# Kernel optimization log

Measured on AMD Instinct MI355X. Metric: run time of the kernel, lower is better.

## Reference

```python
import jax, jax.numpy as jnp
import numpy as np

B, N = 4, 512
C_IN, H, W = 1024, 48, 48
IMG_H, IMG_W = 48.0, 48.0
CNN_EMB, BOX_EMB, GCN_OUT = 512, 256, 512
ROWS, COLS = 58, 30
ALPHA = 5.0
K_EDGES = 8 * N  # edges kept per image per graph

# all directed pairs (i != j) of a fully-connected graph on N nodes
_ii, _jj = np.meshgrid(np.arange(N), np.arange(N), indexing='ij')
_m = _ii != _jj
PAIRS = jnp.asarray(np.stack([_ii[_m], _jj[_m]], axis=1).astype(np.int32))  # [E,2]


def setup_inputs():
    key = jax.random.key(0)
    ks = jax.random.split(key, 12)
    x = jax.random.normal(ks[0], (B, C_IN, H, W), jnp.float32)
    # valid boxes (x1<x2, y1<y2) inside the 48x48 feature map
    p = jax.random.uniform(ks[1], (B, N, 2, 2), minval=0.0, maxval=float(W) - 2.0)
    lo = jnp.min(p, axis=2)
    hi = jnp.max(p, axis=2) + 1.0
    boxes = jnp.concatenate([lo, hi], axis=-1)  # [B,N,4] x1,y1,x2,y2

    def lin(k, fi, fo):
        return jax.random.normal(k, (fi, fo), jnp.float32) / np.sqrt(fi)

    return {
        'input': x, 'boxes': boxes,
        'im_scales': jnp.ones((B,), jnp.float32),
        'pdls': jnp.zeros((B,), jnp.float32),
        'pdts': jnp.zeros((B,), jnp.float32),
        'W_dec': jax.random.normal(ks[2], (256, C_IN, 3, 3), jnp.float32) / np.sqrt(C_IN * 9.0),
        'b_dec': jnp.zeros((256,), jnp.float32),
        'W_box': lin(ks[3], 4, BOX_EMB), 'b_box': jnp.zeros((BOX_EMB,), jnp.float32),
        'W_cnn': lin(ks[4], 256 * 4, CNN_EMB), 'b_cnn': jnp.zeros((CNN_EMB,), jnp.float32),
        'W_grow': lin(ks[5], CNN_EMB + BOX_EMB, GCN_OUT), 'b_grow': jnp.zeros((GCN_OUT,), jnp.float32),
        'W_gcol': lin(ks[6], CNN_EMB + BOX_EMB, GCN_OUT), 'b_gcol': jnp.zeros((GCN_OUT,), jnp.float32),
        'W_rcls': lin(ks[7], GCN_OUT, 2 * (ROWS - 1) * 2), 'b_rcls': jnp.zeros((2 * (ROWS - 1) * 2,), jnp.float32),
        'W_ccls': lin(ks[8], GCN_OUT, 2 * (COLS - 1) * 2), 'b_ccls': jnp.zeros((2 * (COLS - 1) * 2,), jnp.float32),
    }


def _bilinear(feat, bidx, py, px):
    # feat [B,C,H,W]; py,px [M,4] sample coords -> [M,4,C]
    Hh, Ww = feat.shape[2], feat.shape[3]
    py = jnp.clip(py, 0.0, Hh - 1.0)
    px = jnp.clip(px, 0.0, Ww - 1.0)
    y0 = jnp.floor(py).astype(jnp.int32)
    x0 = jnp.floor(px).astype(jnp.int32)
    y1 = jnp.minimum(y0 + 1, Hh - 1)
    x1 = jnp.minimum(x0 + 1, Ww - 1)
    wy = (py - y0)[..., None]
    wx = (px - x0)[..., None]
    b = bidx[:, None]
    f00 = feat[b, :, y0, x0]
    f01 = feat[b, :, y0, x1]
    f10 = feat[b, :, y1, x0]
    f11 = feat[b, :, y1, x1]
    return f00 * (1 - wy) * (1 - wx) + f01 * (1 - wy) * wx + f10 * wy * (1 - wx) + f11 * wy * wx


def _roi_align_2x2(feat, boxes, bidx):
    # roi_align output_size=2, spatial_scale=1, one sample per bin (bin center)
    x1, y1, x2, y2 = boxes[:, 0], boxes[:, 1], boxes[:, 2], boxes[:, 3]
    bw = (x2 - x1) / 2.0
    bh = (y2 - y1) / 2.0
    offs = jnp.array([0.5, 1.5], jnp.float32)
    sx = x1[:, None] + offs * bw[:, None]  # [M,2]
    sy = y1[:, None] + offs * bh[:, None]
    py = sy[:, jnp.array([0, 0, 1, 1])]  # (iy, ix) ordering
    px = sx[:, jnp.array([0, 1, 0, 1])]
    val = _bilinear(feat, bidx, py, px)  # [M,4,C]
    return jnp.transpose(val, (0, 2, 1)).reshape(val.shape[0], -1)  # [M, C*2*2]


def _edge_attrs(boxes_i, scale, pdl, pdt):
    org = (boxes_i - jnp.stack([pdl, pdt, pdl, pdt])) / scale
    cx = (org[:, 0] + org[:, 2]) * 0.5
    cy = (org[:, 1] + org[:, 3]) * 0.5
    tb_w = jnp.max(org[:, jnp.array([0, 2])])
    tb_h = jnp.max(org[:, jnp.array([1, 3])])
    s, d = PAIRS[:, 0], PAIRS[:, 1]
    row_attr = jnp.exp(-jnp.square((cy[s] - cy[d]) * ALPHA / tb_h))
    col_attr = jnp.exp(-jnp.square((cx[s] - cx[d]) * ALPHA / tb_w))
    rv, ri = jax.lax.top_k(row_attr, K_EDGES)
    cv, ci = jax.lax.top_k(col_attr, K_EDGES)
    return rv, PAIRS[ri], cv, PAIRS[ci]


def _gcn(x, Wg, bg, edges, ew, num_nodes):
    # PyG GCNConv: self-loops with weight 1, symmetric normalization
    loop = jnp.arange(num_nodes, dtype=edges.dtype)
    src = jnp.concatenate([edges[0], loop])
    dst = jnp.concatenate([edges[1], loop])
    w = jnp.concatenate([ew, jnp.ones((num_nodes,), ew.dtype)])
    deg = jax.ops.segment_sum(w, dst, num_segments=num_nodes)
    dis = jax.lax.rsqrt(deg)  # deg >= 1 thanks to self-loops
    norm = dis[src] * w * dis[dst]
    xw = x @ Wg
    agg = jax.ops.segment_sum(norm[:, None] * xw[src], dst, num_segments=num_nodes)
    return agg + bg


def _forward(input, boxes, im_scales, pdls, pdts, W_dec, b_dec, W_box, b_box,
             W_cnn, b_cnn, W_grow, b_grow, W_gcol, b_gcol, W_rcls, b_rcls, W_ccls, b_ccls):
    Bn = B * N
    flat = boxes.reshape(Bn, 4)
    # box features (relative center / size)
    cx = (flat[:, 0] + flat[:, 2]) / 2.0
    cy = (flat[:, 1] + flat[:, 3]) / 2.0
    bf = jnp.stack([cx / IMG_W, cy / IMG_H,
                    (flat[:, 2] - flat[:, 0]) / IMG_W,
                    (flat[:, 3] - flat[:, 1]) / IMG_H], axis=1)
    box_feat = jax.nn.relu(bf @ W_box + b_box)
    # decode conv + relu
    dec = jax.lax.conv_general_dilated(input, W_dec, (1, 1), 'SAME',
                                       dimension_numbers=('NCHW', 'OIHW', 'NCHW'))
    dec = jax.nn.relu(dec + b_dec[None, :, None, None])
    # roi-align 2x2 + cnn embedding
    bidx = jnp.repeat(jnp.arange(B, dtype=jnp.int32), N)
    cnn = _roi_align_2x2(dec, flat, bidx)
    cnn_feat = jax.nn.relu(cnn @ W_cnn + b_cnn)
    # per-image dense graph -> top-8N row/col edges
    rv, re, cv, ce = jax.vmap(_edge_attrs)(boxes, im_scales, pdls, pdts)
    off = (jnp.arange(B, dtype=jnp.int32) * N)[:, None, None]
    row_edge = (re + off).reshape(-1, 2).T  # [2, B*K]
    col_edge = (ce + off).reshape(-1, 2).T
    row_w = rv.reshape(-1)
    col_w = cv.reshape(-1)
    fusion = jnp.concatenate([box_feat, cnn_feat], axis=1)  # [Bn, 768]
    row_feat = jax.nn.relu(_gcn(fusion, W_grow, b_grow, row_edge, row_w, Bn))
    col_feat = jax.nn.relu(_gcn(fusion, W_gcol, b_gcol, col_edge, col_w, Bn))
    row_score = jax.nn.leaky_relu(row_feat @ W_rcls + b_rcls, 0.01).reshape(Bn, 2, ROWS - 1, 2)
    col_score = jax.nn.leaky_relu(col_feat @ W_ccls + b_ccls, 0.01).reshape(Bn, 2, COLS - 1, 2)
    return row_score, col_score


def reference(input, boxes, im_scales, pdls, pdts, W_dec, b_dec, W_box, b_box,
              W_cnn, b_cnn, W_grow, b_grow, W_gcol, b_gcol, W_rcls, b_rcls, W_ccls, b_ccls):
    return _forward(input, boxes, im_scales, pdls, pdts, W_dec, b_dec, W_box, b_box,
                    W_cnn, b_cnn, W_grow, b_grow, W_gcol, b_gcol,
                    W_rcls, b_rcls, W_ccls, b_ccls)
```

## Files before the change

### kernel.cpp

```cpp
#include <hip/hip_runtime.h>
#include <cstdint>
#include <math.h>

typedef unsigned int u32;
typedef unsigned long long u64;
typedef unsigned short ushort;

typedef __attribute__((ext_vector_type(8))) _Float16 f16x8;
typedef __attribute__((ext_vector_type(4))) _Float16 f16x4;
typedef __attribute__((ext_vector_type(4))) float f32x4;

#define NB    4
#define BnN   2048
#define NE    261632
#define NCHUNK 16
#define ECHUNK 16352
#define KEDGE 4096
#define TIECAP 2048
#define PSLICE 2359296
#define MS    64
#define TS    64

__global__ __launch_bounds__(256) void cvt_x_kernel(
    const float* __restrict__ in, _Float16* __restrict__ xf)
{
    __shared__ _Float16 sh[64][49];
    int cg = blockIdx.x, y = blockIdx.y, b = blockIdx.z;
    int tid = threadIdx.x;
    for (int i = tid; i < 64 * 48; i += 256) {
        int cl = i / 48, x = i - cl * 48;
        sh[cl][x] = (_Float16)in[(((size_t)b * 1024 + cg * 64 + cl) * 48 + y) * 48 + x];
    }
    __syncthreads();
    for (int i = tid; i < 64 * 48; i += 256) {
        int x = i / 64, cl = i - x * 64;
        xf[((size_t)(b * 48 + y) * 48 + x) * 1024 + cg * 64 + cl] = sh[cl][x];
    }
}

__global__ __launch_bounds__(256) void cvt_w_kernel(
    const float* __restrict__ W, _Float16* __restrict__ wf)
{
    __shared__ _Float16 sh[9216];
    int o = blockIdx.x, tid = threadIdx.x;
    for (int g = tid; g < 9216; g += 256)
        sh[g] = (_Float16)W[(size_t)o * 9216 + g];
    __syncthreads();
    for (int g = tid; g < 9216; g += 256) {
        int tap = g >> 10, ch = g & 1023;
        wf[(size_t)o * 9216 + g] = sh[ch * 9 + tap];
    }
}

__global__ __launch_bounds__(256) void cvt_t5_kernel(
    const float* __restrict__ Wc,  _Float16* __restrict__ WcT,
    const float* __restrict__ Wgr, _Float16* __restrict__ WgrT,
    const float* __restrict__ Wgc, _Float16* __restrict__ WgcT,
    const float* __restrict__ Wr,  _Float16* __restrict__ WrT,
    const float* __restrict__ Wcc, _Float16* __restrict__ WccT)
{
    __shared__ _Float16 sh[32][33];
    int bid = blockIdx.x;
    const float* in; _Float16* out; int K, N, tx0, ty0, ntx;
    if (bid < 512)       { in = Wc;  out = WcT;  K = 1024; N = 512; ntx = 16; bid -= 0;    }
    else if (bid < 896)  { in = Wgr; out = WgrT; K = 768;  N = 512; ntx = 16; bid -= 512;  }
    else if (bid < 1280) { in = Wgc; out = WgcT; K = 768;  N = 512; ntx = 16; bid -= 896;  }
    else if (bid < 1408) { in = Wr;  out = WrT;  K = 512;  N = 228; ntx = 8;  bid -= 1280; }
    else                 { in = Wcc; out = WccT; K = 512;  N = 116; ntx = 4;  bid -= 1408; }
    tx0 = (bid % ntx) * 32;
    ty0 = (bid / ntx) * 32;
    int tx = threadIdx.x & 31, ty = threadIdx.x >> 5;
#pragma unroll
    for (int i = 0; i < 4; ++i) {
        int k = ty0 + ty + i * 8, n = tx0 + tx;
        sh[ty + i * 8][tx] = (k < K && n < N) ? (_Float16)in[(size_t)k * N + n] : (_Float16)0.f;
    }
    __syncthreads();
#pragma unroll
    for (int i = 0; i < 4; ++i) {
        int n = tx0 + ty + i * 8, k = ty0 + tx;
        if (n < N && k < K) out[(size_t)n * K + k] = sh[tx][ty + i * 8];
    }
}

__global__ __launch_bounds__(256) void conv_part_kernel(
    const _Float16* __restrict__ xf, const _Float16* __restrict__ wf,
    float* __restrict__ pbuf)
{
    __shared__ _Float16 wS[9][4][32][8];
    __shared__ _Float16 xS[10][4][50][8];
    const int y0 = blockIdx.x * 8;
    const int og = blockIdx.y;
    const int bz = blockIdx.z;
    const int b  = bz >> 2, ks = bz & 3;
    const int tid = threadIdx.x;
    const int wv = tid >> 6;
    const int ln = tid & 63;
    const int n  = ln & 15;
    const int q  = ln >> 4;

    f32x4 acc[2][2][3];
#pragma unroll
    for (int mt = 0; mt < 2; ++mt)
#pragma unroll
        for (int rr = 0; rr < 2; ++rr)
#pragma unroll
            for (int nt = 0; nt < 3; ++nt) acc[mt][rr][nt] = (f32x4){0.f, 0.f, 0.f, 0.f};

    const int c0 = ks * 256;
    for (int cc = c0; cc < c0 + 256; cc += 32) {
#pragma unroll
        for (int it = 0; it < 5; ++it) {
            int g = it * 256 + tid;
            if (g < 1152) {
                int tap = g >> 7, r = g & 127, qq = r >> 5, oc = r & 31;
                *(uint4*)&wS[tap][qq][oc][0] =
                    *(const uint4*)(wf + ((size_t)(og * 32 + oc) * 9 + tap) * 1024 + cc + qq * 8);
            }
        }
#pragma unroll
        for (int it = 0; it < 8; ++it) {
            int g = it * 256 + tid;
            if (g < 2000) {
                int row = g / 200, r2 = g - row * 200;
                int qq = r2 / 50, c = r2 - qq * 50;
                int gy = y0 + row - 1, gx = c - 1;
                uint4 v = make_uint4(0u, 0u, 0u, 0u);
                if ((unsigned)gy < 48u && (unsigned)gx < 48u)
                    v = *(const uint4*)(xf + ((size_t)(b * 48 + gy) * 48 + gx) * 1024 + cc + qq * 8);
                *(uint4*)&xS[row][qq][c][0] = v;
            }
        }
        __syncthreads();

#pragma unroll
        for (int tap = 0; tap < 9; ++tap) {
            const int dy = tap / 3, dx = tap % 3;
            f16x8 a0 = *(const f16x8*)&wS[tap][q][n][0];
            f16x8 a1 = *(const f16x8*)&wS[tap][q][16 + n][0];
#pragma unroll
            for (int rr = 0; rr < 2; ++rr) {
                const int row = 2 * wv + rr + dy;
#pragma unroll
                for (int nt = 0; nt < 3; ++nt) {
                    f16x8 bb = *(const f16x8*)&xS[row][q][nt * 16 + n + dx][0];
                    acc[0][rr][nt] = __builtin_amdgcn_mfma_f32_16x16x32_f16(a0, bb, acc[0][rr][nt], 0, 0, 0);
                    acc[1][rr][nt] = __builtin_amdgcn_mfma_f32_16x16x32_f16(a1, bb, acc[1][rr][nt], 0, 0, 0);
                }
            }
        }
        __syncthreads();
    }

#pragma unroll
    for (int rr = 0; rr < 2; ++rr) {
        const int y = y0 + 2 * wv + rr;
#pragma unroll
        for (int mt = 0; mt < 2; ++mt) {
#pragma unroll
            for (int nt = 0; nt < 3; ++nt) {
                int x = nt * 16 + n;
                *(f32x4*)(pbuf + (size_t)ks * PSLICE +
                          ((size_t)(b * 48 + y) * 48 + x) * 256 + og * 32 + mt * 16 + q * 4) = acc[mt][rr][nt];
            }
        }
    }
}

__global__ __launch_bounds__(256) void conv_sum_kernel(
    const float* __restrict__ pbuf, const float* __restrict__ bd,
    _Float16* __restrict__ dec)
{
    size_t idx = (size_t)blockIdx.x * 256 + threadIdx.x;
    size_t e = idx * 4;
    int och = (int)(e & 255);
    f32x4 s0 = *(const f32x4*)(pbuf + e);
    f32x4 s1 = *(const f32x4*)(pbuf + (size_t)PSLICE + e);
    f32x4 s2 = *(const f32x4*)(pbuf + (size_t)2 * PSLICE + e);
    f32x4 s3 = *(const f32x4*)(pbuf + (size_t)3 * PSLICE + e);
    float4 b4 = *(const float4*)(bd + och);
    f16x4 v;
    v.x = (_Float16)fmaxf(s0[0] + s1[0] + s2[0] + s3[0] + b4.x, 0.f);
    v.y = (_Float16)fmaxf(s0[1] + s1[1] + s2[1] + s3[1] + b4.y, 0.f);
    v.z = (_Float16)fmaxf(s0[2] + s1[2] + s2[2] + s3[2] + b4.z, 0.f);
    v.w = (_Float16)fmaxf(s0[3] + s1[3] + s2[3] + s3[3] + b4.w, 0.f);
    *(f16x4*)(dec + e) = v;
}

__global__ __launch_bounds__(256) void roi_box_kernel(
    const _Float16* __restrict__ dec, const float* __restrict__ boxes,
    const float* __restrict__ Wb, const float* __restrict__ bb,
    _Float16* __restrict__ cnn, _Float16* __restrict__ fusion)
{
    int n = blockIdx.x; int c = threadIdx.x;
    int b = n >> 9;
    float x1 = boxes[n * 4 + 0], y1 = boxes[n * 4 + 1];
    float x2 = boxes[n * 4 + 2], y2 = boxes[n * 4 + 3];
    {
        float bf0 = ((x1 + x2) * 0.5f) / 48.f;
        float bf1 = ((y1 + y2) * 0.5f) / 48.f;
        float bf2 = (x2 - x1) / 48.f;
        float bf3 = (y2 - y1) / 48.f;
        float acc = bb[c];
        acc += bf0 * Wb[0 * 256 + c];
        acc += bf1 * Wb[1 * 256 + c];
        acc += bf2 * Wb[2 * 256 + c];
        acc += bf3 * Wb[3 * 256 + c];
        fusion[(size_t)n * 768 + c] = (_Float16)fmaxf(acc, 0.f);
    }
    float bw = (x2 - x1) * 0.5f, bh = (y2 - y1) * 0.5f;
    float sxv[2] = { x1 + 0.5f * bw, x1 + 1.5f * bw };
    float syv[2] = { y1 + 0.5f * bh, y1 + 1.5f * bh };
    float px[4] = { sxv[0], sxv[1], sxv[0], sxv[1] };
    float py[4] = { syv[0], syv[0], syv[1], syv[1] };
    const _Float16* f = dec + (size_t)b * 2304 * 256;
    f16x4 o4;
    float res[4];
#pragma unroll
    for (int p = 0; p < 4; ++p) {
        float yy = fminf(fmaxf(py[p], 0.f), 47.f);
        float xx = fminf(fmaxf(px[p], 0.f), 47.f);
        int y0 = (int)floorf(yy), x0 = (int)floorf(xx);
        int y1i = min(y0 + 1, 47), x1i = min(x0 + 1, 47);
        float wy = yy - (float)y0, wx = xx - (float)x0;
        float f00 = (float)f[(size_t)(y0 * 48 + x0) * 256 + c];
        float f01 = (float)f[(size_t)(y0 * 48 + x1i) * 256 + c];
        float f10 = (float)f[(size_t)(y1i * 48 + x0) * 256 + c];
        float f11 = (float)f[(size_t)(y1i * 48 + x1i) * 256 + c];
        res[p] = f00 * (1.f - wy) * (1.f - wx) + f01 * (1.f - wy) * wx
               + f10 * wy * (1.f - wx) + f11 * wy * wx;
    }
    o4.x = (_Float16)res[0]; o4.y = (_Float16)res[1];
    o4.z = (_Float16)res[2]; o4.w = (_Float16)res[3];
    *(f16x4*)(cnn + (size_t)n * 1024 + c * 4) = o4;
}

template <int ACT, typename OUTT>
__global__ __launch_bounds__(256) void gemm16_kernel(
    const _Float16* __restrict__ A, const _Float16* __restrict__ Bt,
    const float* __restrict__ bias, OUTT* __restrict__ C,
    int M, int N, int K, int ldC)
{
    __shared__ _Float16 aS[64][4][8];
    __shared__ _Float16 bS[64][4][8];
    const int n0 = blockIdx.x * 64, m0 = blockIdx.y * 64;
    const int tid = threadIdx.x;
    const int wv = tid >> 6, ln = tid & 63;
    const int wm = wv & 1, wn = wv >> 1;
    const int lm = ln & 15, lq = ln >> 4;
    const int sr = tid >> 2, sq = tid & 3;

    f32x4 acc[2][2];
#pragma unroll
    for (int i = 0; i < 2; ++i)
#pragma unroll
        for (int j = 0; j < 2; ++j) acc[i][j] = (f32x4){0.f, 0.f, 0.f, 0.f};

    for (int cc = 0; cc < K; cc += 32) {
        *(uint4*)&aS[sr][sq][0] = *(const uint4*)(A + (size_t)(m0 + sr) * K + cc + sq * 8);
        uint4 bv = make_uint4(0u, 0u, 0u, 0u);
        if (n0 + sr < N)
            bv = *(const uint4*)(Bt + (size_t)(n0 + sr) * K + cc + sq * 8);
        *(uint4*)&bS[sr][sq][0] = bv;
        __syncthreads();
        f16x8 af[2], bf[2];
#pragma unroll
        for (int mt = 0; mt < 2; ++mt) af[mt] = *(const f16x8*)&aS[wm * 32 + mt * 16 + lm][lq][0];
#pragma unroll
        for (int nt = 0; nt < 2; ++nt) bf[nt] = *(const f16x8*)&bS[wn * 32 + nt * 16 + lm][lq][0];
#pragma unroll
        for (int mt = 0; mt < 2; ++mt)
#pragma unroll
            for (int nt = 0; nt < 2; ++nt)
                acc[mt][nt] = __builtin_amdgcn_mfma_f32_16x16x32_f16(af[mt], bf[nt], acc[mt][nt], 0, 0, 0);
        __syncthreads();
    }

#pragma unroll
    for (int mt = 0; mt < 2; ++mt) {
#pragma unroll
        for (int nt = 0; nt < 2; ++nt) {
            int col = n0 + wn * 32 + nt * 16 + lm;
            if (col >= N) continue;
            float bs = bias ? bias[col] : 0.f;
#pragma unroll
            for (int r = 0; r < 4; ++r) {
                int row = m0 + wm * 32 + mt * 16 + lq * 4 + r;
                float v = acc[mt][nt][r] + bs;
                if (ACT == 1) v = fmaxf(v, 0.f);
                if (ACT == 2) v = (v >= 0.f) ? v : 0.01f * v;
                C[(size_t)row * ldC + col] = (OUTT)v;
            }
        }
    }
}

__global__ __launch_bounds__(256) void gemm16z_kernel(
    const _Float16* __restrict__ A,
    const _Float16* __restrict__ Bt0, const _Float16* __restrict__ Bt1,
    float* __restrict__ C0, float* __restrict__ C1,
    int M, int N, int K, int ldC)
{
    const _Float16* __restrict__ Bt = blockIdx.z ? Bt1 : Bt0;
    float* __restrict__ C = blockIdx.z ? C1 : C0;
    __shared__ _Float16 aS[64][4][8];
    __shared__ _Float16 bS[64][4][8];
    const int n0 = blockIdx.x * 64, m0 = blockIdx.y * 64;
    const int tid = threadIdx.x;
    const int wv = tid >> 6, ln = tid & 63;
    const int wm = wv & 1, wn = wv >> 1;
    const int lm = ln & 15, lq = ln >> 4;
    const int sr = tid >> 2, sq = tid & 3;

    f32x4 acc[2][2];
#pragma unroll
    for (int i = 0; i < 2; ++i)
#pragma unroll
        for (int j = 0; j < 2; ++j) acc[i][j] = (f32x4){0.f, 0.f, 0.f, 0.f};

    for (int cc = 0; cc < K; cc += 32) {
        *(uint4*)&aS[sr][sq][0] = *(const uint4*)(A + (size_t)(m0 + sr) * K + cc + sq * 8);
        uint4 bv = make_uint4(0u, 0u, 0u, 0u);
        if (n0 + sr < N)
            bv = *(const uint4*)(Bt + (size_t)(n0 + sr) * K + cc + sq * 8);
        *(uint4*)&bS[sr][sq][0] = bv;
        __syncthreads();
        f16x8 af[2], bf[2];
#pragma unroll
        for (int mt = 0; mt < 2; ++mt) af[mt] = *(const f16x8*)&aS[wm * 32 + mt * 16 + lm][lq][0];
#pragma unroll
        for (int nt = 0; nt < 2; ++nt) bf[nt] = *(const f16x8*)&bS[wn * 32 + nt * 16 + lm][lq][0];
#pragma unroll
        for (int mt = 0; mt < 2; ++mt)
#pragma unroll
            for (int nt = 0; nt < 2; ++nt)
                acc[mt][nt] = __builtin_amdgcn_mfma_f32_16x16x32_f16(af[mt], bf[nt], acc[mt][nt], 0, 0, 0);
        __syncthreads();
    }

#pragma unroll
    for (int mt = 0; mt < 2; ++mt) {
#pragma unroll
        for (int nt = 0; nt < 2; ++nt) {
            int col = n0 + wn * 32 + nt * 16 + lm;
            if (col >= N) continue;
#pragma unroll
            for (int r = 0; r < 4; ++r) {
                int row = m0 + wm * 32 + mt * 16 + lq * 4 + r;
                C[(size_t)row * ldC + col] = acc[mt][nt][r];
            }
        }
    }
}

__device__ __forceinline__ float compute_sv_tb(
    const float* __restrict__ boxes, const float* __restrict__ scales,
    const float* __restrict__ pdls, const float* __restrict__ pdts,
    int b, int t, float* sv, float* red)
{
    int tid = threadIdx.x;
    float pdl = pdls[b], pdt = pdts[b], sc = scales[b];
    if (tid < 512) {
        const float* bx = boxes + (size_t)(b * 512 + tid) * 4;
        float o0 = (bx[0] - pdl) / sc;
        float o1 = (bx[1] - pdt) / sc;
        float o2 = (bx[2] - pdl) / sc;
        float o3 = (bx[3] - pdt) / sc;
        sv[tid]  = (t == 0) ? (o1 + o3) * 0.5f : (o0 + o2) * 0.5f;
        red[tid] = (t == 0) ? fmaxf(o1, o3)    : fmaxf(o0, o2);
    }
    __syncthreads();
    for (int s = 256; s > 0; s >>= 1) {
        if (tid < s) red[tid] = fmaxf(red[tid], red[tid + s]);
        __syncthreads();
    }
    float tbv = red[0];
    __syncthreads();
    return tbv;
}

#define QBITS(e, QB)                                                   \
    {                                                                  \
        int i_ = (e) / 511; int jj_ = (e) - i_ * 511;                  \
        int j_ = jj_ + (jj_ >= i_ ? 1 : 0);                            \
        float diff_ = sv[i_] - sv[j_];                                 \
        float u_ = (diff_ * 5.0f) / tbv;                               \
        float q_ = u_ * u_;                                            \
        QB = __float_as_uint(q_);                                      \
    }

__global__ __launch_bounds__(1024) void histA_kernel(
    const float* __restrict__ boxes, const float* __restrict__ scales,
    const float* __restrict__ pdls, const float* __restrict__ pdts,
    u32* __restrict__ gpart)
{
    __shared__ float sv[512]; __shared__ float red[512];
    __shared__ u32 lh[4096];
    const int sel = blockIdx.y, b = sel >> 1, t = sel & 1;
    const int tid = threadIdx.x;
    for (int i = tid; i < 4096; i += 1024) lh[i] = 0;
    const float tbv = compute_sv_tb(boxes, scales, pdls, pdts, b, t, sv, red);
    const int e1 = min((int)(blockIdx.x + 1) * ECHUNK, NE);
    for (int e = blockIdx.x * ECHUNK + tid; e < e1; e += 1024) {
        u32 qb; QBITS(e, qb);
        atomicAdd(&lh[qb >> 20], 1u);
    }
    __syncthreads();
    u32* G = gpart + ((size_t)sel * NCHUNK + blockIdx.x) * 4096;
    for (int i = tid; i < 4096; i += 1024) G[i] = lh[i];
}

__global__ __launch_bounds__(1024) void scanA_kernel(
    const u32* __restrict__ gpart, u32* __restrict__ meta)
{
    const int sel = blockIdx.x, tid = threadIdx.x;
    __shared__ u32 bins[4096];
    __shared__ u32 sc[2][1024];
    for (int b = tid; b < 4096; b += 1024) {
        u32 s = 0;
        for (int c = 0; c < NCHUNK; ++c) s += gpart[((size_t)sel * NCHUNK + c) * 4096 + b];
        bins[b] = s;
    }
    __syncthreads();
    u32 part = 0;
#pragma unroll
    for (int j = 0; j < 4; ++j) part += bins[tid * 4 + j];
    sc[0][tid] = part;
    __syncthreads();
    int src = 0;
    for (int st = 1; st < 1024; st <<= 1) {
        sc[1 - src][tid] = sc[src][tid] + (tid >= st ? sc[src][tid - st] : 0);
        __syncthreads(); src = 1 - src;
    }
    u32 inc = sc[src][tid], exc = inc - part;
    if (exc < (u32)KEDGE && (u32)KEDGE <= inc) {
        u32 cum = exc;
        for (int j = 0; j < 4; ++j) {
            u32 c = bins[tid * 4 + j];
            if (cum + c >= (u32)KEDGE) {
                meta[sel * MS + 0] = (u32)(tid * 4 + j);
                meta[sel * MS + 1] = (u32)KEDGE - cum;
                break;
            }
            cum += c;
        }
    }
}

__global__ __launch_bounds__(1024) void histB_kernel(
    const float* __restrict__ boxes, const float* __restrict__ scales,
    const float* __restrict__ pdls, const float* __restrict__ pdts,
    const u32* __restrict__ meta, u32* __restrict__ gpart)
{
    __shared__ float sv[512]; __shared__ float red[512];
    __shared__ u32 lh[4096];
    const int sel = blockIdx.y, b = sel >> 1, t = sel & 1;
    const int tid = threadIdx.x;
    for (int i = tid; i < 4096; i += 1024) lh[i] = 0;
    const float tbv = compute_sv_tb(boxes, scales, pdls, pdts, b, t, sv, red);
    const u32 p12 = meta[sel * MS + 0];
    const int e1 = min((int)(blockIdx.x + 1) * ECHUNK, NE);
    for (int e = blockIdx.x * ECHUNK + tid; e < e1; e += 1024) {
        u32 qb; QBITS(e, qb);
        if ((qb >> 20) == p12) atomicAdd(&lh[(qb >> 8) & 0xFFF], 1u);
    }
    __syncthreads();
    u32* G = gpart + ((size_t)sel * NCHUNK + blockIdx.x) * 4096;
    for (int i = tid; i < 4096; i += 1024) G[i] = lh[i];
}

__global__ __launch_bounds__(1024) void scanB_kernel(
    const u32* __restrict__ gpart, u32* __restrict__ meta)
{
    const int sel = blockIdx.x, tid = threadIdx.x;
    const u32 TH = meta[sel * MS + 1];
    __shared__ u32 bins[4096];
    __shared__ u32 sc[2][1024];
    for (int b = tid; b < 4096; b += 1024) {
        u32 s = 0;
        for (int c = 0; c < NCHUNK; ++c) s += gpart[((size_t)sel * NCHUNK + c) * 4096 + b];
        bins[b] = s;
    }
    __syncthreads();
    u32 part = 0;
#pragma unroll
    for (int j = 0; j < 4; ++j) part += bins[tid * 4 + j];
    sc[0][tid] = part;
    __syncthreads();
    int src = 0;
    for (int st = 1; st < 1024; st <<= 1) {
        sc[1 - src][tid] = sc[src][tid] + (tid >= st ? sc[src][tid - st] : 0);
        __syncthreads(); src = 1 - src;
    }
    u32 inc = sc[src][tid], exc = inc - part;
    if (exc < TH && TH <= inc) {
        u32 cum = exc;
        for (int j = 0; j < 4; ++j) {
            u32 c = bins[tid * 4 + j];
            if (cum + c >= TH) {
                meta[sel * MS + 6] = (meta[sel * MS + 0] << 12) | (u32)(tid * 4 + j);
                meta[sel * MS + 7] = TH - cum;
                break;
            }
            cum += c;
        }
    }
}

__global__ __launch_bounds__(1024) void histC_kernel(
    const float* __restrict__ boxes, const float* __restrict__ scales,
    const float* __restrict__ pdls, const float* __restrict__ pdts,
    const u32* __restrict__ meta, u32* __restrict__ gpart)
{
    __shared__ float sv[512]; __shared__ float red[512];
    __shared__ u32 lh[256];
    const int sel = blockIdx.y, b = sel >> 1, t = sel & 1;
    const int tid = threadIdx.x;
    if (tid < 256) lh[tid] = 0;
    const float tbv = compute_sv_tb(boxes, scales, pdls, pdts, b, t, sv, red);
    const u32 p24 = meta[sel * MS + 6];
    const int e1 = min((int)(blockIdx.x + 1) * ECHUNK, NE);
    for (int e = blockIdx.x * ECHUNK + tid; e < e1; e += 1024) {
        u32 qb; QBITS(e, qb);
        if ((qb >> 8) == p24) atomicAdd(&lh[qb & 0xFF], 1u);
    }
    __syncthreads();
    u32* G = gpart + ((size_t)sel * NCHUNK + blockIdx.x) * 256;
    if (tid < 256) G[tid] = lh[tid];
}

__global__ __launch_bounds__(256) void scanC_kernel(
    const u32* __restrict__ gpart, u32* __restrict__ meta)
{
    const int sel = blockIdx.x, tid = threadIdx.x;
    const u32 TH = meta[sel * MS + 7];
    __shared__ u32 bins[256];
    __shared__ u32 sc[2][256];
    __shared__ u32 s_qstar;
    u32 s = 0;
    for (int c = 0; c < NCHUNK; ++c) s += gpart[((size_t)sel * NCHUNK + c) * 256 + tid];
    bins[tid] = s;
    sc[0][tid] = s;
    __syncthreads();
    int src = 0;
    for (int st = 1; st < 256; st <<= 1) {
        sc[1 - src][tid] = sc[src][tid] + (tid >= st ? sc[src][tid - st] : 0);
        __syncthreads(); src = 1 - src;
    }
    u32 inc = sc[src][tid], exc = inc - bins[tid];
    if (exc < TH && TH <= inc)
        s_qstar = (meta[sel * MS + 6] << 8) | (u32)tid;
    __syncthreads();
    if (tid == 0) {
        u32 prefix = s_qstar;
        float qstar = __uint_as_float(prefix);
        float wstar = (float)exp(-(double)qstar);
        u32 lo = 0, hi = prefix;
        while (lo < hi) {
            u32 mid = (lo + hi) >> 1;
            float wm = (float)exp(-(double)__uint_as_float(mid));
            if (wm > wstar) lo = mid + 1; else hi = mid;
        }
        meta[sel * MS + 2] = lo;
        lo = prefix; hi = 0x7F800000u;
        while (lo < hi) {
            u32 mid = (lo + hi + 1) >> 1;
            float wm = (float)exp(-(double)__uint_as_float(mid));
            if (wm < wstar) hi = mid - 1; else lo = mid;
        }
        meta[sel * MS + 3] = lo;
        meta[sel * MS + 4] = __float_as_uint(wstar);
    }
}

__global__ __launch_bounds__(1024) void emit_kernel(
    const float* __restrict__ boxes, const float* __restrict__ scales,
    const float* __restrict__ pdls, const float* __restrict__ pdts,
    u32* __restrict__ meta, int* __restrict__ tiebuf, int* __restrict__ tiecnt,
    int* __restrict__ es, int* __restrict__ ed, float* __restrict__ ewt,
    int* __restrict__ indeg, float* __restrict__ degw)
{
    __shared__ float sv[512]; __shared__ float red[512];
    __shared__ int s_wcnt, s_tcnt, s_wbase, s_tbase;
    const int sel = blockIdx.y, b = sel >> 1, t = sel & 1;
    const int tid = threadIdx.x;
    const float tbv = compute_sv_tb(boxes, scales, pdls, pdts, b, t, sv, red);
    const u32 qlo = meta[sel * MS + 2], qhi = meta[sel * MS + 3];
    const int base = t * 16384 + b * 4096;
    const int e0 = blockIdx.x * ECHUNK + tid;
    const int e1 = min((int)(blockIdx.x + 1) * ECHUNK, NE);
    if (tid == 0) { s_wcnt = 0; s_tcnt = 0; }
    __syncthreads();
    int myw = 0, myt = 0;
    for (int e = e0; e < e1; e += 1024) {
        u32 qb; QBITS(e, qb);
        if (qb < qlo) ++myw;
        else if (qb <= qhi) ++myt;
    }
    if (myw) atomicAdd(&s_wcnt, myw);
    if (myt) atomicAdd(&s_tcnt, myt);
    __syncthreads();
    if (tid == 0) {
        s_wbase = (s_wcnt > 0) ? (int)atomicAdd(&meta[sel * MS + 5], (u32)s_wcnt) : 0;
        s_tbase = (s_tcnt > 0) ? atomicAdd(&tiecnt[sel * TS], s_tcnt) : 0;
        s_wcnt = 0; s_tcnt = 0;
    }
    __syncthreads();
    for (int e = e0; e < e1; e += 1024) {
        u32 qb; QBITS(e, qb);
        if (qb < qlo) {
            int i = e / 511; int jj = e - i * 511; int j = jj + (jj >= i ? 1 : 0);
            float wval = (float)exp(-(double)__uint_as_float(qb));
            int slot = s_wbase + atomicAdd(&s_wcnt, 1);
            es[base + slot] = b * 512 + i;
            ed[base + slot] = b * 512 + j;
            ewt[base + slot] = wval;
            atomicAdd(&indeg[t * 2048 + b * 512 + j], 1);
            atomicAdd(&degw[t * 2048 + b * 512 + j], wval);
        } else if (qb <= qhi) {
            int p = s_tbase + atomicAdd(&s_tcnt, 1);
            if (p < TIECAP) tiebuf[sel * TIECAP + p] = e;
        }
    }
}

__global__ __launch_bounds__(1024) void tie_scan_fill_kernel(
    u32* __restrict__ meta, const int* __restrict__ tiebuf, const int* __restrict__ tiecnt,
    int* __restrict__ es, int* __restrict__ ed, float* __restrict__ ewt,
    int* __restrict__ indeg, float* __restrict__ degw,
    int* __restrict__ offs, float* __restrict__ dis, int* __restrict__ csr)
{
    __shared__ int bufA[2048], bufB[2048];
    __shared__ int fill_l[2048];
    const int t = blockIdx.x, tid = threadIdx.x;
    for (int b = 0; b < 4; ++b) {
        int sel = b * 2 + t;
        int m = min(tiecnt[sel * TS], TIECAP);
        int r = KEDGE - (int)meta[sel * MS + 5];
        float wt = __uint_as_float(meta[sel * MS + 4]);
        int base = t * 16384 + b * 4096;
        for (int k = tid; k < m; k += 1024) {
            int e = tiebuf[sel * TIECAP + k];
            int rank = 0;
            for (int l = 0; l < m; ++l) rank += (tiebuf[sel * TIECAP + l] < e) ? 1 : 0;
            if (rank < r) {
                int i = e / 511; int jj = e - i * 511; int j = jj + (jj >= i ? 1 : 0);
                int slot = (int)atomicAdd(&meta[sel * MS + 5], 1u);
                es[base + slot] = b * 512 + i;
                ed[base + slot] = b * 512 + j;
                ewt[base + slot] = wt;
                atomicAdd(&indeg[t * 2048 + b * 512 + j], 1);
                atomicAdd(&degw[t * 2048 + b * 512 + j], wt);
            }
        }
    }
    __threadfence();
    __syncthreads();
    bufA[tid] = indeg[t * 2048 + tid];
    bufA[tid + 1024] = indeg[t * 2048 + tid + 1024];
    fill_l[tid] = 0; fill_l[tid + 1024] = 0;
    __syncthreads();
    int* src = bufA; int* dst = bufB;
    for (int st = 1; st < 2048; st <<= 1) {
        dst[tid] = src[tid] + (tid >= st ? src[tid - st] : 0);
        int k1 = tid + 1024;
        dst[k1] = src[k1] + (k1 >= st ? src[k1 - st] : 0);
        __syncthreads();
        int* tmp = src; src = dst; dst = tmp;
    }
    int off0 = (tid == 0) ? 0 : src[tid - 1];
    int off1 = src[tid + 1023];
    __syncthreads();
    dst[tid] = off0; dst[tid + 1024] = off1;
    offs[t * 2048 + tid] = off0;
    offs[t * 2048 + tid + 1024] = off1;
    dis[t * 2048 + tid] = 1.0f / sqrtf(1.0f + degw[t * 2048 + tid]);
    dis[t * 2048 + tid + 1024] = 1.0f / sqrtf(1.0f + degw[t * 2048 + tid + 1024]);
    __syncthreads();
    for (int e = tid; e < 16384; e += 1024) {
        int dl = ed[t * 16384 + e] & 2047;
        int pos = dst[dl] + atomicAdd(&fill_l[dl], 1);
        csr[t * 16384 + pos] = e;
    }
}

__global__ __launch_bounds__(256) void gcn_agg_kernel(
    const float* __restrict__ xw_row, const float* __restrict__ xw_col,
    const float* __restrict__ b_row, const float* __restrict__ b_col,
    const int* __restrict__ es, const float* __restrict__ ew,
    const int* __restrict__ csr, const int* __restrict__ offs,
    const int* __restrict__ indeg, const float* __restrict__ dis,
    _Float16* __restrict__ feat_row, _Float16* __restrict__ feat_col)
{
    int d = blockIdx.x; int t = blockIdx.y;
    const float* xw = t ? xw_col : xw_row;
    const float* bg = t ? b_col : b_row;
    _Float16* out = t ? feat_col : feat_row;
    int f0 = threadIdx.x, f1 = threadIdx.x + 256;
    float dd = dis[t * 2048 + d];
    float a0 = dd * dd * xw[(size_t)d * 512 + f0];
    float a1 = dd * dd * xw[(size_t)d * 512 + f1];
    int st = offs[t * 2048 + d], cnt = indeg[t * 2048 + d];
    for (int k = 0; k < cnt; ++k) {
        int e = csr[t * 16384 + st + k];
        int s = es[t * 16384 + e];
        float w = ew[t * 16384 + e];
        float coef = dis[t * 2048 + s] * w * dd;
        a0 += coef * xw[(size_t)s * 512 + f0];
        a1 += coef * xw[(size_t)s * 512 + f1];
    }
    a0 += bg[f0]; a1 += bg[f1];
    out[(size_t)d * 512 + f0] = (_Float16)fmaxf(a0, 0.f);
    out[(size_t)d * 512 + f1] = (_Float16)fmaxf(a1, 0.f);
}

extern "C" void kernel_launch(void* const* d_in, const int* in_sizes, int n_in,
                              void* d_out, int out_size, void* d_ws, size_t ws_size,
                              hipStream_t stream)
{
    const float* x      = (const float*)d_in[0];
    const float* boxes  = (const float*)d_in[1];
    const float* scales = (const float*)d_in[2];
    const float* pdls   = (const float*)d_in[3];
    const float* pdts   = (const float*)d_in[4];
    const float* W_dec  = (const float*)d_in[5];
    const float* b_dec  = (const float*)d_in[6];
    const float* W_box  = (const float*)d_in[7];
    const float* b_box  = (const float*)d_in[8];
    const float* W_cnn  = (const float*)d_in[9];
    const float* b_cnn  = (const float*)d_in[10];
    const float* W_grow = (const float*)d_in[11];
    const float* b_grow = (const float*)d_in[12];
    const float* W_gcol = (const float*)d_in[13];
    const float* b_gcol = (const float*)d_in[14];
    const float* W_rcls = (const float*)d_in[15];
    const float* b_rcls = (const float*)d_in[16];
    const float* W_ccls = (const float*)d_in[17];
    const float* b_ccls = (const float*)d_in[18];

    char* ws = (char*)d_ws;
    size_t off = 0;
    auto alloc = [&](size_t bytes) -> void* {
        void* p = ws + off;
        off = (off + bytes + 255) & ~(size_t)255;
        return p;
    };
    _Float16* xf16   = (_Float16*)alloc((size_t)4 * 2304 * 1024 * 2);
    _Float16* wf16   = (_Float16*)alloc((size_t)256 * 9216 * 2);
    _Float16* dec    = (_Float16*)alloc((size_t)4 * 2304 * 256 * 2);
    float*    pbuf   = (float*)   alloc((size_t)4 * PSLICE * 4);
    _Float16* cnn    = (_Float16*)alloc((size_t)2048 * 1024 * 2);
    _Float16* fusion = (_Float16*)alloc((size_t)2048 * 768 * 2);
    _Float16* WcT    = (_Float16*)alloc((size_t)512 * 1024 * 2);
    _Float16* WgrT   = (_Float16*)alloc((size_t)512 * 768 * 2);
    _Float16* WgcT   = (_Float16*)alloc((size_t)512 * 768 * 2);
    _Float16* WrT    = (_Float16*)alloc((size_t)228 * 512 * 2);
    _Float16* WccT   = (_Float16*)alloc((size_t)116 * 512 * 2);
    float* xw        = (float*)alloc((size_t)2097152 * 4);
    _Float16* feats  = (_Float16*)alloc((size_t)2 * 2048 * 512 * 2);
    int*  es     = (int*)  alloc((size_t)2 * 16384 * 4);
    int*  ed     = (int*)  alloc((size_t)2 * 16384 * 4);
    float* ewt   = (float*)alloc((size_t)2 * 16384 * 4);
    int*  offsA  = (int*)  alloc((size_t)4096 * 4);
    float* dis   = (float*)alloc((size_t)4096 * 4);
    int*  csr    = (int*)  alloc((size_t)2 * 16384 * 4);
    int*  tiebuf = (int*)  alloc((size_t)8 * TIECAP * 4);
    u32*  gpartA = (u32*)  alloc((size_t)8 * NCHUNK * 4096 * 4);
    u32*  gpartB = (u32*)  alloc((size_t)8 * NCHUNK * 4096 * 4);
    u32*  gpartC = (u32*)  alloc((size_t)8 * NCHUNK * 256 * 4);
    size_t z0 = off;
    u32*  meta   = (u32*)  alloc((size_t)8 * MS * 4);
    int*  tiecnt = (int*)  alloc((size_t)8 * TS * 4);
    int*  indeg  = (int*)  alloc((size_t)4096 * 4);
    float* degw  = (float*)alloc((size_t)4096 * 4);
    size_t z1 = off;

    float* out = (float*)d_out;

    hipMemsetAsync(ws + z0, 0, z1 - z0, stream);

    cvt_x_kernel<<<dim3(16, 48, 4), 256, 0, stream>>>(x, xf16);
    cvt_w_kernel<<<256, 256, 0, stream>>>(W_dec, wf16);
    conv_part_kernel<<<dim3(6, 8, 16), 256, 0, stream>>>(xf16, wf16, pbuf);
    conv_sum_kernel<<<2304, 256, 0, stream>>>(pbuf, b_dec, dec);
    roi_box_kernel<<<2048, 256, 0, stream>>>(dec, boxes, W_box, b_box, cnn, fusion);
    cvt_t5_kernel<<<1472, 256, 0, stream>>>(W_cnn, WcT, W_grow, WgrT, W_gcol, WgcT,
                                            W_rcls, WrT, W_ccls, WccT);
    gemm16_kernel<1, _Float16><<<dim3(8, 32), 256, 0, stream>>>(cnn, WcT, b_cnn, fusion + 256, 2048, 512, 1024, 768);
    histA_kernel<<<dim3(NCHUNK, 8), 1024, 0, stream>>>(boxes, scales, pdls, pdts, gpartA);
    scanA_kernel<<<8, 1024, 0, stream>>>(gpartA, meta);
    histB_kernel<<<dim3(NCHUNK, 8), 1024, 0, stream>>>(boxes, scales, pdls, pdts, meta, gpartB);
    scanB_kernel<<<8, 1024, 0, stream>>>(gpartB, meta);
    histC_kernel<<<dim3(NCHUNK, 8), 1024, 0, stream>>>(boxes, scales, pdls, pdts, meta, gpartC);
    scanC_kernel<<<8, 256, 0, stream>>>(gpartC, meta);
    emit_kernel<<<dim3(NCHUNK, 8), 1024, 0, stream>>>(boxes, scales, pdls, pdts, meta,
                                                      tiebuf, tiecnt, es, ed, ewt, indeg, degw);
    tie_scan_fill_kernel<<<2, 1024, 0, stream>>>(meta, tiebuf, tiecnt, es, ed, ewt,
                                                 indeg, degw, offsA, dis, csr);
    gemm16z_kernel<<<dim3(8, 32, 2), 256, 0, stream>>>(fusion, WgrT, WgcT, xw, xw + 1048576,
                                                       2048, 512, 768, 512);
    gcn_agg_kernel<<<dim3(2048, 2), 256, 0, stream>>>(xw, xw + 1048576, b_grow, b_gcol,
                                                      es, ewt, csr, offsA, indeg, dis,
                                                      feats, feats + (size_t)2048 * 512);
    gemm16_kernel<2, float><<<dim3(4, 32), 256, 0, stream>>>(feats, WrT, b_rcls, out, 2048, 228, 512, 228);
    gemm16_kernel<2, float><<<dim3(2, 32), 256, 0, stream>>>(feats + (size_t)2048 * 512, WccT, b_ccls,
                                                             out + (size_t)2048 * 228, 2048, 116, 512, 116);
}
```

Measured before the change: 374.6 us.

## Software-pipeline conv global loads through registers and remap block order

The conv partial kernel now prefetches the next 32-channel chunk of weights and input into registers while the MFMAs for the current chunk run, then stores them to LDS after a barrier. Global offsets and bounds masks are precomputed once per thread instead of every iteration. The grid is flattened and remapped so consecutive blocks land on different XCDs, the weight tile row is padded to 34 to reduce LDS bank conflicts, and s_setprio raises priority around the MFMA section with a 3-blocks-per-CU launch bound. The cost is higher register pressure from the 13 held uint4 values and an extra barrier per iteration.

```diff
diff --git a/kernel.cpp b/kernel.cpp
--- a/kernel.cpp
+++ b/kernel.cpp
@@ -83,15 +83,51 @@
     }
 }
 
-__global__ __launch_bounds__(256) void conv_part_kernel(
+#define CONV_LOAD(cc)                                                        \
+    {                                                                        \
+        _Pragma("unroll")                                                    \
+        for (int it = 0; it < 5; ++it)                                       \
+            wr[it] = *(const uint4*)(wf + woff[it] + (cc));                  \
+        _Pragma("unroll")                                                    \
+        for (int it = 0; it < 8; ++it)                                       \
+            xr[it] = *(const uint4*)(xf + xoff[it] + (cc));                  \
+    }
+
+#define CONV_STORE()                                                         \
+    {                                                                        \
+        _Pragma("unroll")                                                    \
+        for (int it = 0; it < 5; ++it) {                                     \
+            int g = it * 256 + tid;                                          \
+            if (g < 1152) {                                                  \
+                int tap = g >> 7, r = g & 127, qq = r >> 5, oc = r & 31;     \
+                *(uint4*)&wS[tap][qq][oc][0] = wr[it];                       \
+            }                                                                \
+        }                                                                    \
+        _Pragma("unroll")                                                    \
+        for (int it = 0; it < 8; ++it) {                                     \
+            int g = it * 256 + tid;                                          \
+            if (g < 2000) {                                                  \
+                int row = g / 200, r2 = g - row * 200;                       \
+                int qq = r2 / 50, c = r2 - qq * 50;                          \
+                uint4 v = (xin >> it & 1u) ? xr[it] : make_uint4(0u, 0u, 0u, 0u); \
+                *(uint4*)&xS[row][qq][c][0] = v;                             \
+            }                                                                \
+        }                                                                    \
+    }
+
+__global__ __launch_bounds__(256, 3) void conv_part_kernel(
     const _Float16* __restrict__ xf, const _Float16* __restrict__ wf,
     float* __restrict__ pbuf)
 {
-    __shared__ _Float16 wS[9][4][32][8];
+    __shared__ _Float16 wS[9][4][34][8];
     __shared__ _Float16 xS[10][4][50][8];
-    const int y0 = blockIdx.x * 8;
-    const int og = blockIdx.y;
-    const int bz = blockIdx.z;
+    const int p = blockIdx.x;
+    const int L = (p & 7) * 96 + (p >> 3);
+    const int og = L & 7;
+    const int t  = L >> 3;
+    const int xt = t % 6;
+    const int bz = t / 6;
+    const int y0 = xt * 8;
     const int b  = bz >> 2, ks = bz & 3;
     const int tid = threadIdx.x;
     const int wv = tid >> 6;
@@ -107,32 +143,40 @@
 #pragma unroll
             for (int nt = 0; nt < 3; ++nt) acc[mt][rr][nt] = (f32x4){0.f, 0.f, 0.f, 0.f};
 
+    u32 woff[5];
+    u32 xoff[8];
+    u32 xin = 0;
+#pragma unroll
+    for (int it = 0; it < 5; ++it) {
+        int g = it * 256 + tid;
+        int gg = (g < 1152) ? g : 0;
+        int tap = gg >> 7, r = gg & 127, qq = r >> 5, oc = r & 31;
+        woff[it] = (u32)(((og * 32 + oc) * 9 + tap) * 1024 + qq * 8);
+    }
+#pragma unroll
+    for (int it = 0; it < 8; ++it) {
+        int g = it * 256 + tid;
+        int gg = (g < 2000) ? g : 0;
+        int row = gg / 200, r2 = gg - row * 200;
+        int qq = r2 / 50, c = r2 - qq * 50;
+        int gy = y0 + row - 1, gx = c - 1;
+        bool inb = (g < 2000) && ((unsigned)gy < 48u) && ((unsigned)gx < 48u);
+        if (inb) xin |= (1u << it);
+        xoff[it] = inb ? (u32)(((b * 48 + gy) * 48 + gx) * 1024 + qq * 8) : 0u;
+    }
+
     const int c0 = ks * 256;
-    for (int cc = c0; cc < c0 + 256; cc += 32) {
-#pragma unroll
-        for (int it = 0; it < 5; ++it) {
-            int g = it * 256 + tid;
-            if (g < 1152) {
-                int tap = g >> 7, r = g & 127, qq = r >> 5, oc = r & 31;
-                *(uint4*)&wS[tap][qq][oc][0] =
-                    *(const uint4*)(wf + ((size_t)(og * 32 + oc) * 9 + tap) * 1024 + cc + qq * 8);
-            }
-        }
-#pragma unroll
-        for (int it = 0; it < 8; ++it) {
-            int g = it * 256 + tid;
-            if (g < 2000) {
-                int row = g / 200, r2 = g - row * 200;
-                int qq = r2 / 50, c = r2 - qq * 50;
-                int gy = y0 + row - 1, gx = c - 1;
-                uint4 v = make_uint4(0u, 0u, 0u, 0u);
-                if ((unsigned)gy < 48u && (unsigned)gx < 48u)
-                    v = *(const uint4*)(xf + ((size_t)(b * 48 + gy) * 48 + gx) * 1024 + cc + qq * 8);
-                *(uint4*)&xS[row][qq][c][0] = v;
-            }
-        }
-        __syncthreads();
-
+    uint4 wr[5], xr[8];
+
+    CONV_LOAD(c0);
+    CONV_STORE();
+    __syncthreads();
+
+#pragma unroll 1
+    for (int ci = 0; ci < 8; ++ci) {
+        if (ci < 7) CONV_LOAD(c0 + (ci + 1) * 32);
+
+        __builtin_amdgcn_s_setprio(1);
 #pragma unroll
         for (int tap = 0; tap < 9; ++tap) {
             const int dy = tap / 3, dx = tap % 3;
@@ -149,7 +193,12 @@
                 }
             }
         }
+        __builtin_amdgcn_s_setprio(0);
         __syncthreads();
+        if (ci < 7) {
+            CONV_STORE();
+            __syncthreads();
+        }
     }
 
 #pragma unroll
@@ -781,7 +830,7 @@
 
     cvt_x_kernel<<<dim3(16, 48, 4), 256, 0, stream>>>(x, xf16);
     cvt_w_kernel<<<256, 256, 0, stream>>>(W_dec, wf16);
-    conv_part_kernel<<<dim3(6, 8, 16), 256, 0, stream>>>(xf16, wf16, pbuf);
+    conv_part_kernel<<<dim3(768), 256, 0, stream>>>(xf16, wf16, pbuf);
     conv_sum_kernel<<<2304, 256, 0, stream>>>(pbuf, b_dec, dec);
     roi_box_kernel<<<2048, 256, 0, stream>>>(dec, boxes, W_box, b_box, cnn, fusion);
     cvt_t5_kernel<<<1472, 256, 0, stream>>>(W_cnn, WcT, W_grow, WgrT, W_gcol, WgcT,
```

After: 399.3 us. 6.6% more time.

## Load conv tiles with global_load_lds and remap block order for locality

Applied to the files above, without the earlier changes.

The conv partial kernel now stages weight and input tiles straight from global memory into LDS with the global_load_lds builtin, which removes the register round-trip. Per-thread source pointers are precomputed once, and out-of-bounds halo loads read from a zeroed buffer. A 1D grid with a swizzled block index groups the blocks that share weights, and s_setprio raises wave priority during the MFMA phase. Loads are still fully waited on before compute, so little overlap is added, and the zero buffer lives in a region that is memset every run.

```diff
diff --git a/kernel.cpp b/kernel.cpp
--- a/kernel.cpp
+++ b/kernel.cpp
@@ -83,15 +83,36 @@
     }
 }
 
+#define GLD16(gsrc, ldst)                                                    \
+    __builtin_amdgcn_global_load_lds(                                        \
+        (const __attribute__((address_space(1))) void*)(gsrc),               \
+        (__attribute__((address_space(3))) void*)(ldst), 16, 0, 0)
+
+#define STAGE(cc)                                                            \
+    {                                                                        \
+        _Pragma("unroll")                                                    \
+        for (int it = 0; it < 5; ++it) {                                     \
+            if (it * 256 + wv * 64 < 1152)                                   \
+                GLD16(wsrc[it] + (cc), &wS[(it * 256 + wv * 64) * 8]);       \
+        }                                                                    \
+        _Pragma("unroll")                                                    \
+        for (int it = 0; it < 8; ++it)                                       \
+            GLD16(xsrc[it] + (cc), &xS[(it * 256 + wv * 64) * 8]);           \
+    }
+
 __global__ __launch_bounds__(256) void conv_part_kernel(
     const _Float16* __restrict__ xf, const _Float16* __restrict__ wf,
-    float* __restrict__ pbuf)
-{
-    __shared__ _Float16 wS[9][4][32][8];
-    __shared__ _Float16 xS[10][4][50][8];
-    const int y0 = blockIdx.x * 8;
-    const int og = blockIdx.y;
-    const int bz = blockIdx.z;
+    const _Float16* __restrict__ zbuf, float* __restrict__ pbuf)
+{
+    __shared__ _Float16 wS[1152 * 8];
+    __shared__ _Float16 xS[2048 * 8];
+    const int p = blockIdx.x;
+    const int L = (p & 7) * 96 + (p >> 3);
+    const int og = L & 7;
+    const int t  = L >> 3;
+    const int xt = t % 6;
+    const int bz = t / 6;
+    const int y0 = xt * 8;
     const int b  = bz >> 2, ks = bz & 3;
     const int tid = threadIdx.x;
     const int wv = tid >> 6;
@@ -107,49 +128,54 @@
 #pragma unroll
             for (int nt = 0; nt < 3; ++nt) acc[mt][rr][nt] = (f32x4){0.f, 0.f, 0.f, 0.f};
 
+    const _Float16* wsrc[5];
+    const _Float16* xsrc[8];
+#pragma unroll
+    for (int it = 0; it < 5; ++it) {
+        int g = it * 256 + tid;
+        int gg = (g < 1152) ? g : 0;
+        int tap = gg >> 7, r = gg & 127, qq = r >> 5, oc = r & 31;
+        wsrc[it] = wf + (size_t)(((og * 32 + oc) * 9 + tap) * 1024 + qq * 8);
+    }
+#pragma unroll
+    for (int it = 0; it < 8; ++it) {
+        int g = it * 256 + tid;
+        int row = g / 200, r2 = g - row * 200;
+        int qq = r2 / 50, c = r2 - qq * 50;
+        int gy = y0 + row - 1, gx = c - 1;
+        bool inb = (g < 2000) && ((unsigned)gy < 48u) && ((unsigned)gx < 48u);
+        xsrc[it] = inb ? (xf + (size_t)(((b * 48 + gy) * 48 + gx) * 1024 + qq * 8)) : zbuf;
+    }
+
     const int c0 = ks * 256;
-    for (int cc = c0; cc < c0 + 256; cc += 32) {
-#pragma unroll
-        for (int it = 0; it < 5; ++it) {
-            int g = it * 256 + tid;
-            if (g < 1152) {
-                int tap = g >> 7, r = g & 127, qq = r >> 5, oc = r & 31;
-                *(uint4*)&wS[tap][qq][oc][0] =
-                    *(const uint4*)(wf + ((size_t)(og * 32 + oc) * 9 + tap) * 1024 + cc + qq * 8);
-            }
-        }
-#pragma unroll
-        for (int it = 0; it < 8; ++it) {
-            int g = it * 256 + tid;
-            if (g < 2000) {
-                int row = g / 200, r2 = g - row * 200;
-                int qq = r2 / 50, c = r2 - qq * 50;
-                int gy = y0 + row - 1, gx = c - 1;
-                uint4 v = make_uint4(0u, 0u, 0u, 0u);
-                if ((unsigned)gy < 48u && (unsigned)gx < 48u)
-                    v = *(const uint4*)(xf + ((size_t)(b * 48 + gy) * 48 + gx) * 1024 + cc + qq * 8);
-                *(uint4*)&xS[row][qq][c][0] = v;
-            }
-        }
+
+    STAGE(c0);
+
+#pragma unroll 1
+    for (int ci = 0; ci < 8; ++ci) {
+        asm volatile("s_waitcnt vmcnt(0)" ::: "memory");
         __syncthreads();
 
+        __builtin_amdgcn_s_setprio(1);
 #pragma unroll
         for (int tap = 0; tap < 9; ++tap) {
             const int dy = tap / 3, dx = tap % 3;
-            f16x8 a0 = *(const f16x8*)&wS[tap][q][n][0];
-            f16x8 a1 = *(const f16x8*)&wS[tap][q][16 + n][0];
+            f16x8 a0 = *(const f16x8*)&wS[(tap * 128 + q * 32 + n) * 8];
+            f16x8 a1 = *(const f16x8*)&wS[(tap * 128 + q * 32 + 16 + n) * 8];
 #pragma unroll
             for (int rr = 0; rr < 2; ++rr) {
                 const int row = 2 * wv + rr + dy;
 #pragma unroll
                 for (int nt = 0; nt < 3; ++nt) {
-                    f16x8 bb = *(const f16x8*)&xS[row][q][nt * 16 + n + dx][0];
+                    f16x8 bb = *(const f16x8*)&xS[((row * 4 + q) * 50 + nt * 16 + n + dx) * 8];
                     acc[0][rr][nt] = __builtin_amdgcn_mfma_f32_16x16x32_f16(a0, bb, acc[0][rr][nt], 0, 0, 0);
                     acc[1][rr][nt] = __builtin_amdgcn_mfma_f32_16x16x32_f16(a1, bb, acc[1][rr][nt], 0, 0, 0);
                 }
             }
         }
+        __builtin_amdgcn_s_setprio(0);
         __syncthreads();
+        if (ci < 7) STAGE(c0 + (ci + 1) * 32);
     }
 
 #pragma unroll
@@ -773,6 +799,7 @@
     int*  tiecnt = (int*)  alloc((size_t)8 * TS * 4);
     int*  indeg  = (int*)  alloc((size_t)4096 * 4);
     float* degw  = (float*)alloc((size_t)4096 * 4);
+    _Float16* zbuf = (_Float16*)alloc((size_t)4096);
     size_t z1 = off;
 
     float* out = (float*)d_out;
@@ -781,7 +808,7 @@
 
     cvt_x_kernel<<<dim3(16, 48, 4), 256, 0, stream>>>(x, xf16);
     cvt_w_kernel<<<256, 256, 0, stream>>>(W_dec, wf16);
-    conv_part_kernel<<<dim3(6, 8, 16), 256, 0, stream>>>(xf16, wf16, pbuf);
+    conv_part_kernel<<<dim3(768), 256, 0, stream>>>(xf16, wf16, zbuf, pbuf);
     conv_sum_kernel<<<2304, 256, 0, stream>>>(pbuf, b_dec, dec);
     roi_box_kernel<<<2048, 256, 0, stream>>>(dec, boxes, W_box, b_box, cnn, fusion);
     cvt_t5_kernel<<<1472, 256, 0, stream>>>(W_cnn, WcT, W_grow, WgrT, W_gcol, WgcT,
```

After: 362.7 us. 1.03x faster.
